# Kernel optimization log

Hardware: AMD Instinct MI355X
Metric: run time of the kernel (lower is better)

Reference implementation:

```python
import jax, jax.numpy as jnp
import numpy as np

N_NODES = 100000
IN_CH, HIDDEN, OUT_CH = 128, 64, 40
N_EDGES = 1600000


def gcn_conv(x, row, col, W, b, num_nodes):
    """PyG GCNConv: x' = D^-1/2 (A+I) D^-1/2 (x W) + b, self-loops already in row/col."""
    h = x @ W  # [N, out]
    deg = jax.ops.segment_sum(jnp.ones_like(col, dtype=h.dtype), col, num_segments=num_nodes)
    dinv = jnp.where(deg > 0, jax.lax.rsqrt(deg), 0.0)  # [N]
    norm = dinv[row] * dinv[col]  # [E+N]
    msg = h[row] * norm[:, None]  # gather + scale
    out = jax.ops.segment_sum(msg, col, num_segments=num_nodes)  # scatter-add to targets
    return out + b


def setup_inputs() -> dict:
    key = jax.random.key(0)
    k = jax.random.split(key, 6)
    x = jax.random.normal(k[0], (N_NODES, IN_CH), dtype=jnp.float32)
    ei = jax.random.randint(k[1], (2, N_EDGES), 0, N_NODES, dtype=jnp.int64)
    # Glorot-style init for linear weights, zeros for biases (PyG defaults)
    W1 = jax.random.normal(k[2], (IN_CH, HIDDEN), dtype=jnp.float32) / np.sqrt(IN_CH)
    b1 = jnp.zeros((HIDDEN,), dtype=jnp.float32)
    W2 = jax.random.normal(k[3], (HIDDEN, OUT_CH), dtype=jnp.float32) / np.sqrt(HIDDEN)
    b2 = jnp.zeros((OUT_CH,), dtype=jnp.float32)
    return {"x": x, "ei": ei, "W1": W1, "b1": b1, "W2": W2, "b2": b2}


def reference(x, ei, W1, b1, W2, b2):
    num_nodes = x.shape[0]
    loop = jnp.arange(num_nodes, dtype=ei.dtype)
    row = jnp.concatenate([ei[0], loop])  # sources + self-loops
    col = jnp.concatenate([ei[1], loop])  # targets + self-loops
    h = jax.nn.relu(gcn_conv(x, row, col, W1, b1, num_nodes))
    # dropout(p=0.5) is identity in eval mode (deterministic reference)
    return gcn_conv(h, row, col, W2, b2, num_nodes)
```

## Files before the change

### kernel.cpp

```cpp
#include <hip/hip_runtime.h>
#include <hip/hip_bf16.h>
#include <math.h>

#define IN_CH 128
#define HID 64
#define OUT_CH 40
#define NBUCK 512
#define CAP2 6250
#define CAPL 5120

typedef const __hip_bfloat16* bf16p;
typedef __attribute__((ext_vector_type(8))) short bf16x8;
typedef __attribute__((ext_vector_type(4))) short bf16x4;
typedef __attribute__((ext_vector_type(4))) float f32x4;
typedef __attribute__((ext_vector_type(8))) float f32x8;

__device__ __forceinline__ f32x4 cvt4(bf16x4 v) {
    f32x4 o;
    #pragma unroll
    for (int j = 0; j < 4; ++j) {
        unsigned int bits = ((unsigned int)(unsigned short)v[j]) << 16;
        o[j] = __uint_as_float(bits);
    }
    return o;
}

__device__ __forceinline__ f32x8 cvt8(bf16x8 v) {
    f32x8 o;
    #pragma unroll
    for (int j = 0; j < 8; ++j) {
        unsigned int bits = ((unsigned int)(unsigned short)v[j]) << 16;
        o[j] = __uint_as_float(bits);
    }
    return o;
}

__device__ __forceinline__ bf16x4 pack4(f32x4 v) {
    bf16x4 o;
    #pragma unroll
    for (int j = 0; j < 4; ++j) {
        __hip_bfloat16 b = __float2bfloat16(v[j]);
        o[j] = *reinterpret_cast<short*>(&b);
    }
    return o;
}

__device__ __forceinline__ bf16x8 pack8(f32x8 v) {
    bf16x8 o;
    #pragma unroll
    for (int j = 0; j < 8; ++j) {
        __hip_bfloat16 b = __float2bfloat16(v[j]);
        o[j] = *reinterpret_cast<short*>(&b);
    }
    return o;
}

__device__ __forceinline__ int bucket_of(int c, int N, float invN512) {
    int b = (int)((float)c * invN512);
    long long c512 = (long long)c << 9;
    while ((long long)(b + 1) * N <= c512) ++b;
    while (b > 0 && (long long)b * N > c512) --b;
    return b;
}

__global__ void k_detect(const void* x, const void* ei, int* flags) {
    __shared__ int s_f32, s_hi;
    if (threadIdx.x == 0) { s_f32 = 0; s_hi = 0; }
    __syncthreads();
    const __hip_bfloat16* xb = (const __hip_bfloat16*)x;
    const int* ii = (const int*)ei;
    int lf = 0, lh = 0;
    for (int i = threadIdx.x; i < 4096; i += blockDim.x) {
        float f = __bfloat162float(xb[i]);
        if (!(fabsf(f) <= 1e4f)) lf = 1;
        lh |= ii[2 * i + 1];
    }
    if (lf) atomicOr(&s_f32, 1);
    if (lh) atomicOr(&s_hi, 1);
    __syncthreads();
    if (threadIdx.x == 0) {
        flags[0] = s_f32 ? 1 : 0;
        flags[1] = (s_hi == 0) ? 1 : 0;
        flags[2] = 0;
    }
}

__global__ void k_convw(const void* W1, const void* b1, const void* W2, const void* b2,
                        const int* flags, float* wf) {
    int i = blockIdx.x * blockDim.x + threadIdx.x;
    if (i >= 10856) return;
    const void* src; int off;
    if (i < 8192)       { src = W1; off = i; }
    else if (i < 8256)  { src = b1; off = i - 8192; }
    else if (i < 10816) { src = W2; off = i - 8256; }
    else                { src = b2; off = i - 10816; }
    float v;
    if (flags[0]) v = ((const float*)src)[off];
    else          v = __bfloat162float(((bf16p)src)[off]);
    wf[i] = v;
}

__global__ __launch_bounds__(256) void k_bin2(const int* ei, const int* flags,
        int* bincnt2, long long* bins2, int E, int N, float invN512) {
    __shared__ int cnt[NBUCK], base[NBUCK];
    for (int i = threadIdx.x; i < NBUCK; i += 256) cnt[i] = 0;
    __syncthreads();
    const int i64 = flags[1];
    const int e0 = blockIdx.x * 4096;
    const int e1 = min(e0 + 4096, E);
    for (int e = e0 + threadIdx.x; e < e1; e += 256) {
        int c = i64 ? ei[2 * (E + e)] : ei[E + e];
        atomicAdd(&cnt[bucket_of(c, N, invN512)], 1);
    }
    __syncthreads();
    for (int i = threadIdx.x; i < NBUCK; i += 256) {
        int v = cnt[i];
        base[i] = v ? atomicAdd(&bincnt2[i], v) : 0;
        cnt[i] = 0;
    }
    __syncthreads();
    for (int e = e0 + threadIdx.x; e < e1; e += 256) {
        int r, c;
        if (i64) { r = ei[2 * e]; c = ei[2 * (E + e)]; }
        else     { r = ei[e];     c = ei[E + e]; }
        int b = bucket_of(c, N, invN512);
        int slot = base[b] + atomicAdd(&cnt[b], 1);
        if (slot < CAP2)
            bins2[(size_t)b * CAP2 + slot] = ((long long)r << 32) | (unsigned int)c;
    }
}

__global__ __launch_bounds__(512) void k_scan512(const int* bincnt2, int* gbase) {
    __shared__ int s[NBUCK];
    int tid = threadIdx.x;
    int v = min(bincnt2[tid], CAPL);
    s[tid] = v;
    __syncthreads();
    for (int off = 1; off < NBUCK; off <<= 1) {
        int t = (tid >= off) ? s[tid - off] : 0;
        __syncthreads();
        s[tid] += t;
        __syncthreads();
    }
    gbase[tid] = s[tid] - v;
    if (tid == NBUCK - 1) gbase[NBUCK] = s[tid];
}

__global__ __launch_bounds__(256) void k_csr(const long long* bins2, const int* bincnt2,
        const int* gbase, int* rowstart, float* dinv, int* erow, int N) {
    __shared__ long long rc[CAPL];
    __shared__ int sdeg[256], lcur[256];
    const int s = blockIdx.x;
    const int tid = threadIdx.x;
    const int nlo = (int)(((long long)s * N + 511) >> 9);
    const int nhi = (int)(((long long)(s + 1) * N + 511) >> 9);
    const int width = nhi - nlo;
    const int cnt = min(bincnt2[s], CAPL);
    const int gb = gbase[s];

    for (int i = tid; i < cnt; i += 256) rc[i] = bins2[(size_t)s * CAP2 + i];
    sdeg[tid] = 0;
    __syncthreads();
    for (int i = tid; i < cnt; i += 256) {
        int j = (int)(rc[i] & 0xffffffffLL) - nlo;
        if (j >= 0 && j < width) atomicAdd(&sdeg[j], 1);
    }
    __syncthreads();
    int my = sdeg[tid];
    __syncthreads();
    for (int off = 1; off < 256; off <<= 1) {
        int t = (tid >= off) ? sdeg[tid - off] : 0;
        __syncthreads();
        sdeg[tid] += t;
        __syncthreads();
    }
    int excl = sdeg[tid] - my;
    lcur[tid] = excl;
    if (tid < width) {
        rowstart[nlo + tid] = gb + excl;
        dinv[nlo + tid] = rsqrtf((float)my + 1.0f);
    }
    if (s == NBUCK - 1 && tid == 0) rowstart[N] = gbase[NBUCK];
    __syncthreads();
    for (int i = tid; i < cnt; i += 256) {
        long long v = rc[i];
        int j = (int)(v & 0xffffffffLL) - nlo;
        if (j >= 0 && j < width) {
            int pos = atomicAdd(&lcur[j], 1);
            erow[gb + pos] = (int)(v >> 32);
        }
    }
}

__global__ __launch_bounds__(256) void k_gemm1_mfma(const void* x, const float* W1f,
        __hip_bfloat16* h1b, const int* flags, int N) {
    __shared__ __align__(16) unsigned short wT[HID][IN_CH];
    for (int i = threadIdx.x; i < IN_CH * HID; i += 256) {
        int k = i >> 6, c = i & 63;
        __hip_bfloat16 b = __float2bfloat16(W1f[i]);
        wT[c][k] = *reinterpret_cast<unsigned short*>(&b);
    }
    __syncthreads();

    const int isF32 = flags[0];
    const int lane = threadIdx.x & 63;
    const int wid  = threadIdx.x >> 6;
    const int r = lane & 15;
    const int g = lane >> 4;

    bf16x8 bfr[4][4];
    #pragma unroll
    for (int nt = 0; nt < 4; ++nt)
        #pragma unroll
        for (int ks = 0; ks < 4; ++ks)
            bfr[nt][ks] = *(const bf16x8*)&wT[nt * 16 + r][ks * 32 + g * 8];

    const int tiles = (N + 15) >> 4;
    for (int t = blockIdx.x * 4 + wid; t < tiles; t += gridDim.x * 4) {
        const int row0 = t * 16;
        int arow = row0 + r; if (arow >= N) arow = N - 1;
        bf16x8 afr[4];
        if (!isF32) {
            const unsigned short* xr = (const unsigned short*)x + (size_t)arow * IN_CH;
            #pragma unroll
            for (int ks = 0; ks < 4; ++ks)
                afr[ks] = *(const bf16x8*)&xr[ks * 32 + g * 8];
        } else {
            const float* xr = (const float*)x + (size_t)arow * IN_CH;
            #pragma unroll
            for (int ks = 0; ks < 4; ++ks) {
                #pragma unroll
                for (int j = 0; j < 8; ++j) {
                    __hip_bfloat16 b = __float2bfloat16(xr[ks * 32 + g * 8 + j]);
                    afr[ks][j] = *reinterpret_cast<short*>(&b);
                }
            }
        }
        f32x4 acc[4] = {};
        #pragma unroll
        for (int ks = 0; ks < 4; ++ks)
            #pragma unroll
            for (int nt = 0; nt < 4; ++nt)
                acc[nt] = __builtin_amdgcn_mfma_f32_16x16x32_bf16(afr[ks], bfr[nt][ks],
                                                                  acc[nt], 0, 0, 0);
        #pragma unroll
        for (int nt = 0; nt < 4; ++nt) {
            #pragma unroll
            for (int q = 0; q < 4; ++q) {
                int rr = row0 + g * 4 + q;
                if (rr < N)
                    h1b[(size_t)rr * HID + nt * 16 + r] = __float2bfloat16(acc[nt][q]);
            }
        }
    }
}

__global__ __launch_bounds__(256) void k_agg1(const int* rowstart, const int* erow,
        const __hip_bfloat16* h1b, const float* dinv, const float* b1f,
        __hip_bfloat16* g, int N) {
    const int lane = threadIdx.x & 63;
    const int sub = lane >> 3;
    const int co  = lane & 7;
    const f32x4 b1a = *(const f32x4*)&b1f[co * 8];
    const f32x4 b1b = *(const f32x4*)&b1f[co * 8 + 4];
    const int wstride = (gridDim.x * 256) >> 6;
    for (int w = (blockIdx.x * 256 + threadIdx.x) >> 6; w < N; w += wstride) {
        int s0 = __builtin_amdgcn_readfirstlane(rowstart[w]);
        int s1 = __builtin_amdgcn_readfirstlane(rowstart[w + 1]);
        float d = dinv[w];
        bf16x8 sv = *(const bf16x8*)&h1b[(size_t)w * HID + co * 8];
        f32x8 acc = {};
        int i = s0 + sub;
        for (; i + 8 < s1; i += 16) {
            int r0 = erow[i], r1 = erow[i + 8];
            float n0 = dinv[r0] * d, n1 = dinv[r1] * d;
            f32x8 v0 = cvt8(*(const bf16x8*)&h1b[(size_t)r0 * HID + co * 8]);
            f32x8 v1 = cvt8(*(const bf16x8*)&h1b[(size_t)r1 * HID + co * 8]);
            #pragma unroll
            for (int j = 0; j < 8; ++j) {
                acc[j] = fmaf(v0[j], n0, acc[j]);
                acc[j] = fmaf(v1[j], n1, acc[j]);
            }
        }
        if (i < s1) {
            int r0 = erow[i];
            float n0 = dinv[r0] * d;
            f32x8 v0 = cvt8(*(const bf16x8*)&h1b[(size_t)r0 * HID + co * 8]);
            #pragma unroll
            for (int j = 0; j < 8; ++j) acc[j] = fmaf(v0[j], n0, acc[j]);
        }
        #pragma unroll
        for (int j = 0; j < 8; ++j) {
            acc[j] += __shfl_xor(acc[j], 8);
            acc[j] += __shfl_xor(acc[j], 16);
            acc[j] += __shfl_xor(acc[j], 32);
        }
        if (sub == 0) {
            float dd = d * d;
            f32x8 sf = cvt8(sv);
            f32x8 gv;
            #pragma unroll
            for (int j = 0; j < 4; ++j) {
                gv[j]     = fmaxf(fmaf(sf[j], dd, acc[j]) + b1a[j], 0.f);
                gv[j + 4] = fmaxf(fmaf(sf[j + 4], dd, acc[j + 4]) + b1b[j], 0.f);
            }
            *(bf16x8*)&g[(size_t)w * HID + co * 8] = pack8(gv);
        }
    }
}

__global__ __launch_bounds__(256) void k_agg2s(const int* rowstart, const int* erow,
        const __hip_bfloat16* g, const float* dinv, __hip_bfloat16* sbuf, int N) {
    const int lane = threadIdx.x & 63;
    const int sub = lane >> 3;
    const int co  = lane & 7;
    const int wstride = (gridDim.x * 256) >> 6;
    for (int w = (blockIdx.x * 256 + threadIdx.x) >> 6; w < N; w += wstride) {
        int s0 = __builtin_amdgcn_readfirstlane(rowstart[w]);
        int s1 = __builtin_amdgcn_readfirstlane(rowstart[w + 1]);
        float d = dinv[w];
        bf16x8 sv = *(const bf16x8*)&g[(size_t)w * HID + co * 8];
        f32x8 acc = {};
        int i = s0 + sub;
        for (; i + 8 < s1; i += 16) {
            int r0 = erow[i], r1 = erow[i + 8];
            float n0 = dinv[r0] * d, n1 = dinv[r1] * d;
            f32x8 v0 = cvt8(*(const bf16x8*)&g[(size_t)r0 * HID + co * 8]);
            f32x8 v1 = cvt8(*(const bf16x8*)&g[(size_t)r1 * HID + co * 8]);
            #pragma unroll
            for (int j = 0; j < 8; ++j) {
                acc[j] = fmaf(v0[j], n0, acc[j]);
                acc[j] = fmaf(v1[j], n1, acc[j]);
            }
        }
        if (i < s1) {
            int r0 = erow[i];
            float n0 = dinv[r0] * d;
            f32x8 v0 = cvt8(*(const bf16x8*)&g[(size_t)r0 * HID + co * 8]);
            #pragma unroll
            for (int j = 0; j < 8; ++j) acc[j] = fmaf(v0[j], n0, acc[j]);
        }
        #pragma unroll
        for (int j = 0; j < 8; ++j) {
            acc[j] += __shfl_xor(acc[j], 8);
            acc[j] += __shfl_xor(acc[j], 16);
            acc[j] += __shfl_xor(acc[j], 32);
        }
        if (sub == 0) {
            float dd = d * d;
            f32x8 sf = cvt8(sv);
            f32x8 ov;
            #pragma unroll
            for (int j = 0; j < 8; ++j) ov[j] = fmaf(sf[j], dd, acc[j]);
            *(bf16x8*)&sbuf[(size_t)w * HID + co * 8] = pack8(ov);
        }
    }
}

__global__ __launch_bounds__(256) void k_gemm2_mfma(const __hip_bfloat16* sbuf,
        const float* W2f, const float* b2f, float* out, int N) {
    __shared__ __align__(16) unsigned short w2T[48][HID];
    for (int i = threadIdx.x; i < 48 * HID; i += 256) {
        int c = i >> 6, k = i & 63;
        float v = (c < OUT_CH) ? W2f[k * OUT_CH + c] : 0.f;
        __hip_bfloat16 b = __float2bfloat16(v);
        w2T[c][k] = *reinterpret_cast<unsigned short*>(&b);
    }
    __syncthreads();

    const int lane = threadIdx.x & 63;
    const int wid  = threadIdx.x >> 6;
    const int r = lane & 15;
    const int gq = lane >> 4;

    bf16x8 bfr[3][2];
    #pragma unroll
    for (int nt = 0; nt < 3; ++nt)
        #pragma unroll
        for (int ks = 0; ks < 2; ++ks)
            bfr[nt][ks] = *(const bf16x8*)&w2T[nt * 16 + r][ks * 32 + gq * 8];
    float b2v[3];
    #pragma unroll
    for (int nt = 0; nt < 3; ++nt)
        b2v[nt] = (nt * 16 + r < OUT_CH) ? b2f[nt * 16 + r] : 0.f;

    const int tiles = (N + 15) >> 4;
    for (int t = blockIdx.x * 4 + wid; t < tiles; t += gridDim.x * 4) {
        const int row0 = t * 16;
        int arow = row0 + r; if (arow >= N) arow = N - 1;
        const unsigned short* sr = (const unsigned short*)sbuf + (size_t)arow * HID;
        bf16x8 afr[2];
        afr[0] = *(const bf16x8*)&sr[gq * 8];
        afr[1] = *(const bf16x8*)&sr[32 + gq * 8];
        f32x4 acc[3] = {};
        #pragma unroll
        for (int ks = 0; ks < 2; ++ks)
            #pragma unroll
            for (int nt = 0; nt < 3; ++nt)
                acc[nt] = __builtin_amdgcn_mfma_f32_16x16x32_bf16(afr[ks], bfr[nt][ks],
                                                                  acc[nt], 0, 0, 0);
        #pragma unroll
        for (int nt = 0; nt < 3; ++nt) {
            int c = nt * 16 + r;
            #pragma unroll
            for (int q = 0; q < 4; ++q) {
                int rr = row0 + gq * 4 + q;
                if (rr < N && c < OUT_CH)
                    out[(size_t)rr * OUT_CH + c] = acc[nt][q] + b2v[nt];
            }
        }
    }
}

extern "C" void kernel_launch(void* const* d_in, const int* in_sizes, int n_in,
                              void* d_out, int out_size, void* d_ws, size_t ws_size,
                              hipStream_t stream) {
    const void* x  = d_in[0];
    const void* ei = d_in[1];
    const void* W1 = d_in[2];
    const void* b1 = d_in[3];
    const void* W2 = d_in[4];
    const void* b2 = d_in[5];
    const int N = in_sizes[0] / IN_CH;
    const int E = in_sizes[1] / 2;
    const int* eii = (const int*)ei;

    float* ws = (float*)d_ws;
    size_t off = 16;
    int*   flags    = (int*)ws;
    int*   bincnt2  = (int*)ws + off;            off += NBUCK;
    int*   gbase    = (int*)ws + off;            off += NBUCK + 8;
    float* dinv     = ws + off;                  off += N;
    float* wf       = ws + off;                  off += 10880;
    int*   rowstart = (int*)ws + off;            off += N + 1;
    off = (off + 255) & ~(size_t)255;
    int*   erow     = (int*)ws + off;            off += E;
    off = (off + 255) & ~(size_t)255;
    __hip_bfloat16* h1b = (__hip_bfloat16*)(ws + off);     off += (size_t)N * HID / 2;
    __hip_bfloat16* g   = (__hip_bfloat16*)(ws + off);     off += (size_t)N * HID / 2;
    __hip_bfloat16* sbuf = h1b;
    long long* bins2 = (long long*)h1b;

    hipMemsetAsync(bincnt2, 0, NBUCK * sizeof(int), stream);

    k_detect<<<1, 256, 0, stream>>>(x, ei, flags);
    k_convw<<<(10856 + 255) / 256, 256, 0, stream>>>(W1, b1, W2, b2, flags, wf);

    float invN512 = 512.0f / (float)N;
    int nbin = (E + 4095) / 4096;
    k_bin2<<<nbin, 256, 0, stream>>>(eii, flags, bincnt2, bins2, E, N, invN512);
    k_scan512<<<1, NBUCK, 0, stream>>>(bincnt2, gbase);
    k_csr<<<NBUCK, 256, 0, stream>>>(bins2, bincnt2, gbase, rowstart, dinv, erow, N);

    int tiles = (N + 15) / 16;
    int g1 = (tiles + 7) / 8;
    k_gemm1_mfma<<<g1, 256, 0, stream>>>(x, wf, h1b, flags, N);

    k_agg1<<<2048, 256, 0, stream>>>(rowstart, erow, h1b, dinv, wf + 8192, g, N);
    k_agg2s<<<2048, 256, 0, stream>>>(rowstart, erow, g, dinv, sbuf, N);
    k_gemm2_mfma<<<g1, 256, 0, stream>>>(sbuf, wf + 8256, wf + 10816, (float*)d_out, N);
}
```

Before: 277.8 us.

## Merge setup kernels, drop scan kernel, use 1024 buckets and larger grids

Fuses dtype detection with the weight conversion into one launch. The separate bucket-offset scan kernel is removed; each CSR block instead reduces the counts of the buckets before it. The bucket count doubles to 1024 (bucket width now about 98 nodes), k_bin2 moves to 512 threads with a 4x unrolled counting loop, and the aggregation grids double. Kernel launches drop from two to one for setup and from one for the scan, at the cost of redundant prefix work in every CSR block. With 1024 buckets the per-bucket capacity CAPL=2560 sits much closer to the expected ~1660 edges per bucket, so overflow risk stays moderate.

```diff
diff --git a/kernel.cpp b/kernel.cpp
--- a/kernel.cpp
+++ b/kernel.cpp
@@ -5,25 +5,15 @@
 #define IN_CH 128
 #define HID 64
 #define OUT_CH 40
-#define NBUCK 512
-#define CAP2 6250
-#define CAPL 5120
+#define NBUCK 1024
+#define NBSHIFT 10
+#define CAP2 3125
+#define CAPL 2560
 
 typedef const __hip_bfloat16* bf16p;
 typedef __attribute__((ext_vector_type(8))) short bf16x8;
-typedef __attribute__((ext_vector_type(4))) short bf16x4;
 typedef __attribute__((ext_vector_type(4))) float f32x4;
 typedef __attribute__((ext_vector_type(8))) float f32x8;
-
-__device__ __forceinline__ f32x4 cvt4(bf16x4 v) {
-    f32x4 o;
-    #pragma unroll
-    for (int j = 0; j < 4; ++j) {
-        unsigned int bits = ((unsigned int)(unsigned short)v[j]) << 16;
-        o[j] = __uint_as_float(bits);
-    }
-    return o;
-}
 
 __device__ __forceinline__ f32x8 cvt8(bf16x8 v) {
     f32x8 o;
@@ -35,16 +25,6 @@
     return o;
 }
 
-__device__ __forceinline__ bf16x4 pack4(f32x4 v) {
-    bf16x4 o;
-    #pragma unroll
-    for (int j = 0; j < 4; ++j) {
-        __hip_bfloat16 b = __float2bfloat16(v[j]);
-        o[j] = *reinterpret_cast<short*>(&b);
-    }
-    return o;
-}
-
 __device__ __forceinline__ bf16x8 pack8(f32x8 v) {
     bf16x8 o;
     #pragma unroll
@@ -55,22 +35,24 @@
     return o;
 }
 
-__device__ __forceinline__ int bucket_of(int c, int N, float invN512) {
-    int b = (int)((float)c * invN512);
-    long long c512 = (long long)c << 9;
-    while ((long long)(b + 1) * N <= c512) ++b;
-    while (b > 0 && (long long)b * N > c512) --b;
+__device__ __forceinline__ int bucket_of(int c, int N, float invNB) {
+    int b = (int)((float)c * invNB);
+    long long cB = (long long)c << NBSHIFT;
+    while ((long long)(b + 1) * N <= cB) ++b;
+    while (b > 0 && (long long)b * N > cB) --b;
     return b;
 }
 
-__global__ void k_detect(const void* x, const void* ei, int* flags) {
+__global__ __launch_bounds__(256) void k_detectconv(const void* x, const void* ei,
+        int* flags, const void* W1, const void* b1, const void* W2, const void* b2,
+        float* wf) {
     __shared__ int s_f32, s_hi;
     if (threadIdx.x == 0) { s_f32 = 0; s_hi = 0; }
     __syncthreads();
     const __hip_bfloat16* xb = (const __hip_bfloat16*)x;
     const int* ii = (const int*)ei;
     int lf = 0, lh = 0;
-    for (int i = threadIdx.x; i < 4096; i += blockDim.x) {
+    for (int i = threadIdx.x; i < 4096; i += 256) {
         float f = __bfloat162float(xb[i]);
         if (!(fabsf(f) <= 1e4f)) lf = 1;
         lh |= ii[2 * i + 1];
@@ -78,85 +60,83 @@
     if (lf) atomicOr(&s_f32, 1);
     if (lh) atomicOr(&s_hi, 1);
     __syncthreads();
+    const int isF32 = s_f32 ? 1 : 0;
     if (threadIdx.x == 0) {
-        flags[0] = s_f32 ? 1 : 0;
+        flags[0] = isF32;
         flags[1] = (s_hi == 0) ? 1 : 0;
         flags[2] = 0;
     }
-}
-
-__global__ void k_convw(const void* W1, const void* b1, const void* W2, const void* b2,
-                        const int* flags, float* wf) {
-    int i = blockIdx.x * blockDim.x + threadIdx.x;
-    if (i >= 10856) return;
-    const void* src; int off;
-    if (i < 8192)       { src = W1; off = i; }
-    else if (i < 8256)  { src = b1; off = i - 8192; }
-    else if (i < 10816) { src = W2; off = i - 8256; }
-    else                { src = b2; off = i - 10816; }
-    float v;
-    if (flags[0]) v = ((const float*)src)[off];
-    else          v = __bfloat162float(((bf16p)src)[off]);
-    wf[i] = v;
-}
-
-__global__ __launch_bounds__(256) void k_bin2(const int* ei, const int* flags,
-        int* bincnt2, long long* bins2, int E, int N, float invN512) {
+    for (int i = threadIdx.x; i < 10856; i += 256) {
+        const void* src; int off;
+        if (i < 8192)       { src = W1; off = i; }
+        else if (i < 8256)  { src = b1; off = i - 8192; }
+        else if (i < 10816) { src = W2; off = i - 8256; }
+        else                { src = b2; off = i - 10816; }
+        wf[i] = isF32 ? ((const float*)src)[off]
+                      : __bfloat162float(((bf16p)src)[off]);
+    }
+}
+
+__global__ __launch_bounds__(512) void k_bin2(const int* ei, const int* flags,
+        int* bincnt2, long long* bins2, int E, int N, float invNB) {
     __shared__ int cnt[NBUCK], base[NBUCK];
-    for (int i = threadIdx.x; i < NBUCK; i += 256) cnt[i] = 0;
+    for (int i = threadIdx.x; i < NBUCK; i += 512) cnt[i] = 0;
     __syncthreads();
     const int i64 = flags[1];
     const int e0 = blockIdx.x * 4096;
     const int e1 = min(e0 + 4096, E);
-    for (int e = e0 + threadIdx.x; e < e1; e += 256) {
+    int e = e0 + threadIdx.x;
+    for (; e + 3 * 512 < e1; e += 4 * 512) {
+        int c0 = i64 ? ei[2 * (E + e)]        : ei[E + e];
+        int c1 = i64 ? ei[2 * (E + e + 512)]  : ei[E + e + 512];
+        int c2 = i64 ? ei[2 * (E + e + 1024)] : ei[E + e + 1024];
+        int c3 = i64 ? ei[2 * (E + e + 1536)] : ei[E + e + 1536];
+        atomicAdd(&cnt[bucket_of(c0, N, invNB)], 1);
+        atomicAdd(&cnt[bucket_of(c1, N, invNB)], 1);
+        atomicAdd(&cnt[bucket_of(c2, N, invNB)], 1);
+        atomicAdd(&cnt[bucket_of(c3, N, invNB)], 1);
+    }
+    for (; e < e1; e += 512) {
         int c = i64 ? ei[2 * (E + e)] : ei[E + e];
-        atomicAdd(&cnt[bucket_of(c, N, invN512)], 1);
-    }
-    __syncthreads();
-    for (int i = threadIdx.x; i < NBUCK; i += 256) {
+        atomicAdd(&cnt[bucket_of(c, N, invNB)], 1);
+    }
+    __syncthreads();
+    for (int i = threadIdx.x; i < NBUCK; i += 512) {
         int v = cnt[i];
         base[i] = v ? atomicAdd(&bincnt2[i], v) : 0;
         cnt[i] = 0;
     }
     __syncthreads();
-    for (int e = e0 + threadIdx.x; e < e1; e += 256) {
+    for (e = e0 + threadIdx.x; e < e1; e += 512) {
         int r, c;
         if (i64) { r = ei[2 * e]; c = ei[2 * (E + e)]; }
         else     { r = ei[e];     c = ei[E + e]; }
-        int b = bucket_of(c, N, invN512);
+        int b = bucket_of(c, N, invNB);
         int slot = base[b] + atomicAdd(&cnt[b], 1);
         if (slot < CAP2)
             bins2[(size_t)b * CAP2 + slot] = ((long long)r << 32) | (unsigned int)c;
     }
 }
 
-__global__ __launch_bounds__(512) void k_scan512(const int* bincnt2, int* gbase) {
-    __shared__ int s[NBUCK];
-    int tid = threadIdx.x;
-    int v = min(bincnt2[tid], CAPL);
-    s[tid] = v;
-    __syncthreads();
-    for (int off = 1; off < NBUCK; off <<= 1) {
-        int t = (tid >= off) ? s[tid - off] : 0;
-        __syncthreads();
-        s[tid] += t;
-        __syncthreads();
-    }
-    gbase[tid] = s[tid] - v;
-    if (tid == NBUCK - 1) gbase[NBUCK] = s[tid];
-}
-
 __global__ __launch_bounds__(256) void k_csr(const long long* bins2, const int* bincnt2,
-        const int* gbase, int* rowstart, float* dinv, int* erow, int N) {
+        int* rowstart, float* dinv, int* erow, int N) {
     __shared__ long long rc[CAPL];
-    __shared__ int sdeg[256], lcur[256];
+    __shared__ int sdeg[256], lcur[256], red[256];
     const int s = blockIdx.x;
     const int tid = threadIdx.x;
-    const int nlo = (int)(((long long)s * N + 511) >> 9);
-    const int nhi = (int)(((long long)(s + 1) * N + 511) >> 9);
+    int part = 0;
+    for (int j = tid; j < s; j += 256) part += min(bincnt2[j], CAPL);
+    red[tid] = part;
+    __syncthreads();
+    for (int o = 128; o > 0; o >>= 1) {
+        if (tid < o) red[tid] += red[tid + o];
+        __syncthreads();
+    }
+    const int gb = red[0];
+    const int nlo = (int)(((long long)s * N + NBUCK - 1) >> NBSHIFT);
+    const int nhi = (int)(((long long)(s + 1) * N + NBUCK - 1) >> NBSHIFT);
     const int width = nhi - nlo;
     const int cnt = min(bincnt2[s], CAPL);
-    const int gb = gbase[s];
 
     for (int i = tid; i < cnt; i += 256) rc[i] = bins2[(size_t)s * CAP2 + i];
     sdeg[tid] = 0;
@@ -180,7 +160,7 @@
         rowstart[nlo + tid] = gb + excl;
         dinv[nlo + tid] = rsqrtf((float)my + 1.0f);
     }
-    if (s == NBUCK - 1 && tid == 0) rowstart[N] = gbase[NBUCK];
+    if (s == NBUCK - 1 && tid == 0) rowstart[N] = gb + cnt;
     __syncthreads();
     for (int i = tid; i < cnt; i += 256) {
         long long v = rc[i];
@@ -429,7 +409,6 @@
     size_t off = 16;
     int*   flags    = (int*)ws;
     int*   bincnt2  = (int*)ws + off;            off += NBUCK;
-    int*   gbase    = (int*)ws + off;            off += NBUCK + 8;
     float* dinv     = ws + off;                  off += N;
     float* wf       = ws + off;                  off += 10880;
     int*   rowstart = (int*)ws + off;            off += N + 1;
@@ -443,20 +422,18 @@
 
     hipMemsetAsync(bincnt2, 0, NBUCK * sizeof(int), stream);
 
-    k_detect<<<1, 256, 0, stream>>>(x, ei, flags);
-    k_convw<<<(10856 + 255) / 256, 256, 0, stream>>>(W1, b1, W2, b2, flags, wf);
-
-    float invN512 = 512.0f / (float)N;
+    k_detectconv<<<1, 256, 0, stream>>>(x, ei, flags, W1, b1, W2, b2, wf);
+
+    float invNB = (float)NBUCK / (float)N;
     int nbin = (E + 4095) / 4096;
-    k_bin2<<<nbin, 256, 0, stream>>>(eii, flags, bincnt2, bins2, E, N, invN512);
-    k_scan512<<<1, NBUCK, 0, stream>>>(bincnt2, gbase);
-    k_csr<<<NBUCK, 256, 0, stream>>>(bins2, bincnt2, gbase, rowstart, dinv, erow, N);
+    k_bin2<<<nbin, 512, 0, stream>>>(eii, flags, bincnt2, bins2, E, N, invNB);
+    k_csr<<<NBUCK, 256, 0, stream>>>(bins2, bincnt2, rowstart, dinv, erow, N);
 
     int tiles = (N + 15) / 16;
     int g1 = (tiles + 7) / 8;
     k_gemm1_mfma<<<g1, 256, 0, stream>>>(x, wf, h1b, flags, N);
 
-    k_agg1<<<2048, 256, 0, stream>>>(rowstart, erow, h1b, dinv, wf + 8192, g, N);
-    k_agg2s<<<2048, 256, 0, stream>>>(rowstart, erow, g, dinv, sbuf, N);
+    k_agg1<<<4096, 256, 0, stream>>>(rowstart, erow, h1b, dinv, wf + 8192, g, N);
+    k_agg2s<<<4096, 256, 0, stream>>>(rowstart, erow, g, dinv, sbuf, N);
     k_gemm2_mfma<<<g1, 256, 0, stream>>>(sbuf, wf + 8256, wf + 10816, (float*)d_out, N);
 }
```

New measurement: 269.6 us. -2.9%, faster.
